# Optimization experiments

Measured on AMD Instinct MI355X. Metric: run time of the kernel, lower is better.

## Reference

```python
import jax, jax.numpy as jnp
import numpy as np

B, S, H = 1, 1024, 2048
E, F, FS = 32, 768, 4096
TOP_K = 4
SCALE = 0.02


def setup_inputs() -> dict:
    key = jax.random.key(0)
    ks = jax.random.split(key, 9)
    return {
        "hidden_states": jax.random.normal(ks[0], (B, S, H), jnp.float32),
        "router_weight": jax.random.normal(ks[1], (E, H), jnp.float32) * SCALE,
        "w_gate": jax.random.normal(ks[2], (E, H, F), jnp.float32) * SCALE,
        "w_up": jax.random.normal(ks[3], (E, H, F), jnp.float32) * SCALE,
        "w_down": jax.random.normal(ks[4], (E, F, H), jnp.float32) * SCALE,
        "sw_gate": jax.random.normal(ks[5], (H, FS), jnp.float32) * SCALE,
        "sw_up": jax.random.normal(ks[6], (H, FS), jnp.float32) * SCALE,
        "sw_down": jax.random.normal(ks[7], (FS, H), jnp.float32) * SCALE,
        "sgate_w": jax.random.normal(ks[8], (H, 1), jnp.float32) * SCALE,
    }


def reference(hidden_states, router_weight, w_gate, w_up, w_down,
              sw_gate, sw_up, sw_down, sgate_w):
    b, s, h = hidden_states.shape
    x = hidden_states.reshape(-1, h)                      # [T,H]
    T = x.shape[0]

    # ---- router: linear -> softmax (fp32) -> topk -> renormalize ----
    logits = x @ router_weight.T                          # [T,E]
    probs = jax.nn.softmax(logits.astype(jnp.float32), axis=-1)
    topv, topi = jax.lax.top_k(probs, TOP_K)              # [T,K]
    topv = topv / jnp.sum(topv, axis=-1, keepdims=True)
    topv = topv.astype(probs.dtype)

    # combine weights: scatter topk weights into dense [T,E] mask
    combine = jnp.zeros((T, E), probs.dtype).at[
        jnp.arange(T)[:, None], topi].add(topv)

    # ---- experts: SwiGLU per expert, weighted combine ----
    g = jnp.einsum('th,ehf->etf', x, w_gate)              # [E,T,F]
    u = jnp.einsum('th,ehf->etf', x, w_up)                # [E,T,F]
    act = jax.nn.silu(g) * u                              # [E,T,F]
    out = jnp.einsum('te,etf,efh->th', combine, act, w_down)  # [T,H]

    # ---- shared expert with sigmoid gate ----
    shared = (jax.nn.silu(x @ sw_gate) * (x @ sw_up)) @ sw_down  # [T,H]
    out = out + jax.nn.sigmoid(x @ sgate_w) * shared

    return out.reshape(b, s, h)
```

## Files before the change

kernel.cpp:

```cpp
#include <hip/hip_runtime.h>
#include <math.h>

#define T_TOK 1024
#define H_DIM 2048
#define N_EXP 32
#define TOPK  4
#define F_DIM 768
#define FS_DIM 4096
#define FS_HALF 2048

typedef __bf16 bf16;
typedef __attribute__((ext_vector_type(2))) __bf16 bf16x2;
typedef __attribute__((ext_vector_type(4))) __bf16 bf16x4;
typedef __attribute__((ext_vector_type(8))) __bf16 bf16x8;
typedef __attribute__((ext_vector_type(4))) float f32x4;

#define BAR() do {                                        \
    asm volatile("s_waitcnt lgkmcnt(0)" ::: "memory");    \
    __builtin_amdgcn_s_barrier();                         \
    __builtin_amdgcn_sched_barrier(0);                    \
  } while (0)

__global__ __launch_bounds__(256) void router_kernel(
    const float* __restrict__ x, const float* __restrict__ rw,
    const float* __restrict__ sgw,
    float* __restrict__ topw, float* __restrict__ sg,
    int* __restrict__ counts, int* __restrict__ lists)
{
  int t = blockIdx.x; int tid = threadIdx.x;
  int lane = tid & 63, wave = tid >> 6;
  float acc[N_EXP];
  #pragma unroll
  for (int e = 0; e < N_EXP; e++) acc[e] = 0.f;
  float accs = 0.f;
  const float* xr = x + (size_t)t * H_DIM;
  for (int h = tid; h < H_DIM; h += 256) {
    float xv = xr[h];
    accs += xv * sgw[h];
    #pragma unroll
    for (int e = 0; e < N_EXP; e++) acc[e] += xv * rw[e * H_DIM + h];
  }
  __shared__ float red[4][N_EXP];
  __shared__ float reds[4];
  __shared__ float logits[N_EXP];
  #pragma unroll
  for (int e = 0; e < N_EXP; e++) {
    float v = acc[e];
    for (int off = 32; off; off >>= 1) v += __shfl_down(v, off, 64);
    if (lane == 0) red[wave][e] = v;
  }
  {
    float v = accs;
    for (int off = 32; off; off >>= 1) v += __shfl_down(v, off, 64);
    if (lane == 0) reds[wave] = v;
  }
  __syncthreads();
  if (tid < N_EXP) logits[tid] = red[0][tid] + red[1][tid] + red[2][tid] + red[3][tid];
  __syncthreads();
  if (tid == 0) {
    float m = -1e30f;
    #pragma unroll
    for (int e = 0; e < N_EXP; e++) m = fmaxf(m, logits[e]);
    float p[N_EXP];
    #pragma unroll
    for (int e = 0; e < N_EXP; e++) p[e] = expf(logits[e] - m);
    int ids[TOPK]; float vs[TOPK]; float wsum = 0.f;
    #pragma unroll
    for (int k = 0; k < TOPK; k++) {
      int best = 0; float bv = -1.f;
      for (int e = 0; e < N_EXP; e++) {
        if (p[e] > bv) { bv = p[e]; best = e; }
      }
      ids[k] = best; vs[k] = bv; wsum += bv; p[best] = -2.f;
    }
    float inv = 1.f / wsum;
    float sgs = reds[0] + reds[1] + reds[2] + reds[3];
    sg[t] = 1.f / (1.f + expf(-sgs));
    #pragma unroll
    for (int k = 0; k < TOPK; k++) {
      int slot = t * TOPK + k;
      topw[slot] = vs[k] * inv;
      int pos = atomicAdd(&counts[ids[k]], 1);
      lists[ids[k] * T_TOK + pos] = slot;
    }
  }
}

__global__ __launch_bounds__(256, 4) void gateup_fused(
    const float* __restrict__ X,
    const float* __restrict__ wg_, const float* __restrict__ wu_,
    const float* __restrict__ swg, const float* __restrict__ swu,
    bf16* __restrict__ act, bf16* __restrict__ acts,
    const int* __restrict__ lists, const int* __restrict__ counts,
    int n_shared, int sh_fbs, int actsN, int col_off)
{
  int id = blockIdx.x;
  bool gather = id >= n_shared;
  const float *Wg, *Wu; const int* lb = nullptr;
  int count, mt, fb, ldb, Nout; bf16* C;
  if (gather) {
    int g = id - n_shared;
    int j = g >> 3;
    int e = (g & 7) + 8 * (j / 96);
    int rr = j % 96;
    fb = (rr % 12) * 64; mt = (rr / 12) * 64;
    count = counts[e]; lb = lists + e * T_TOK;
    Wg = wg_ + (size_t)e * H_DIM * F_DIM;
    Wu = wu_ + (size_t)e * H_DIM * F_DIM;
    ldb = F_DIM; Nout = F_DIM; C = act;
  } else {
    fb = (id % sh_fbs) * 64; mt = (id / sh_fbs) * 64;
    count = T_TOK; ldb = FS_DIM; Nout = actsN;
    Wg = swg + col_off; Wu = swu + col_off;
    C = acts;
  }
  if (mt >= count) return;

  int tid = threadIdx.x;
  int lane = tid & 63, wid = tid >> 6;
  int wr = wid >> 1, wc = wid & 1;

  __shared__ alignas(16) bf16 sA [2][64][40];
  __shared__ alignas(16) bf16 sBg[2][64][40];
  __shared__ alignas(16) bf16 sBu[2][64][40];

  const float* aptr;
  {
    int r = mt + (tid >> 2);
    int rc = r < count ? r : count - 1;
    int tok = gather ? (lb[rc] >> 2) : rc;
    aptr = X + (size_t)tok * H_DIM + ((tid & 3) << 3);
  }
  int tid7 = tid & 127;
  int bk4 = (tid7 >> 4) << 2;
  int bng = tid7 & 15;
  const float* bptr = (tid < 128 ? Wg : Wu) + (size_t)bk4 * ldb + fb + bng * 4;

  f32x4 accg[2][2], accu[2][2];
  #pragma unroll
  for (int m = 0; m < 2; m++)
    #pragma unroll
    for (int n = 0; n < 2; n++) {
      accg[m][n] = (f32x4){0.f,0.f,0.f,0.f};
      accu[m][n] = (f32x4){0.f,0.f,0.f,0.f};
    }

  f32x4 avA[2], bvA[4], avB[2], bvB[4];

  #define ISSUE(av, bv, k0) do {                                      \
    av[0] = *(const f32x4*)(aptr + (k0));                             \
    av[1] = *(const f32x4*)(aptr + (k0) + 4);                         \
    _Pragma("unroll")                                                 \
    for (int r_ = 0; r_ < 4; r_++)                                    \
      bv[r_] = *(const f32x4*)(bptr + (size_t)((k0) + r_) * ldb);     \
  } while (0)

  #define STAGE(b, av, bv) do {                                       \
    bf16x8 t8;                                                        \
    _Pragma("unroll")                                                 \
    for (int j_ = 0; j_ < 4; j_++) {                                  \
      t8[j_] = (bf16)av[0][j_]; t8[4 + j_] = (bf16)av[1][j_];         \
    }                                                                 \
    *(bf16x8*)&sA[b][tid >> 2][(tid & 3) << 3] = t8;                  \
    bf16* bdst_ = (tid < 128) ? &sBg[b][0][0] : &sBu[b][0][0];        \
    _Pragma("unroll")                                                 \
    for (int i_ = 0; i_ < 4; i_++) {                                  \
      bf16x4 tb;                                                      \
      tb[0] = (bf16)bv[0][i_]; tb[1] = (bf16)bv[1][i_];               \
      tb[2] = (bf16)bv[2][i_]; tb[3] = (bf16)bv[3][i_];               \
      *(bf16x4*)(bdst_ + (bng * 4 + i_) * 40 + bk4) = tb;             \
    }                                                                 \
  } while (0)

  #define MFMA_PHASE(b) do {                                          \
    int fc = (lane >> 4) << 3;                                        \
    bf16x8 af0 = *(const bf16x8*)&sA[b][wr * 32 + (lane & 15)][fc];   \
    bf16x8 af1 = *(const bf16x8*)&sA[b][wr * 32 + 16 + (lane & 15)][fc]; \
    _Pragma("unroll")                                                 \
    for (int n_ = 0; n_ < 2; n_++) {                                  \
      int nr = wc * 32 + n_ * 16 + (lane & 15);                       \
      bf16x8 bg = *(const bf16x8*)&sBg[b][nr][fc];                    \
      bf16x8 bu = *(const bf16x8*)&sBu[b][nr][fc];                    \
      accg[0][n_] = __builtin_amdgcn_mfma_f32_16x16x32_bf16(af0, bg, accg[0][n_], 0,0,0); \
      accu[0][n_] = __builtin_amdgcn_mfma_f32_16x16x32_bf16(af0, bu, accu[0][n_], 0,0,0); \
      accg[1][n_] = __builtin_amdgcn_mfma_f32_16x16x32_bf16(af1, bg, accg[1][n_], 0,0,0); \
      accu[1][n_] = __builtin_amdgcn_mfma_f32_16x16x32_bf16(af1, bu, accu[1][n_], 0,0,0); \
    }                                                                 \
  } while (0)

  ISSUE(avA, bvA, 0);
  ISSUE(avB, bvB, 32);
  STAGE(0, avA, bvA);
  BAR();
  const int NT = H_DIM / 32;
  for (int t = 0; t < NT; t += 2) {
    if (t + 2 < NT) ISSUE(avA, bvA, (t + 2) * 32);
    MFMA_PHASE(0);
    STAGE(1, avB, bvB);
    BAR();
    if (t + 3 < NT) ISSUE(avB, bvB, (t + 3) * 32);
    MFMA_PHASE(1);
    if (t + 2 < NT) STAGE(0, avA, bvA);
    BAR();
  }
  #undef ISSUE
  #undef STAGE
  #undef MFMA_PHASE

  #pragma unroll
  for (int m = 0; m < 2; m++) {
    #pragma unroll
    for (int q = 0; q < 4; q++) {
      int gr = mt + wr * 32 + m * 16 + (lane >> 4) * 4 + q;
      if (gr < count) {
        size_t rowo = (gather ? (size_t)lb[gr] : (size_t)gr) * Nout;
        #pragma unroll
        for (int n = 0; n < 2; n++) {
          float g = accg[m][n][q], u = accu[m][n][q];
          C[rowo + fb + wc * 32 + n * 16 + (lane & 15)] =
              (bf16)(g / (1.f + __expf(-g)) * u);
        }
      }
    }
  }
}

__global__ __launch_bounds__(256, 4) void down_fused(
    const bf16* __restrict__ act, const bf16* __restrict__ acts,
    const float* __restrict__ wd_, const float* __restrict__ swd,
    bf16* __restrict__ dslot, float* __restrict__ out,
    const float* __restrict__ sg,
    const int* __restrict__ lists, const int* __restrict__ counts,
    int n_shared, int lda_sh, int kd_sh, int swd_off, int accum)
{
  int id = blockIdx.x;
  bool expert = id >= n_shared;
  const bf16* A; const float* W; const int* lb = nullptr;
  int count, mt, nb, Kd, lda;
  if (expert) {
    int g = id - n_shared;
    int j = g >> 3;
    int e = (g & 7) + 8 * (j >> 8);
    int rr = j & 255;
    nb = (rr & 31) * 64; mt = (rr >> 5) * 64;
    count = counts[e]; lb = lists + e * T_TOK;
    A = act; lda = F_DIM; Kd = F_DIM;
    W = wd_ + (size_t)e * F_DIM * H_DIM;
  } else {
    nb = (id & 31) * 64; mt = (id >> 5) * 64;
    count = T_TOK; A = acts; lda = lda_sh; Kd = kd_sh;
    W = swd + (size_t)swd_off * H_DIM;
  }
  if (mt >= count) return;

  int tid = threadIdx.x;
  int lane = tid & 63, wid = tid >> 6;
  int wr = wid >> 1, wc = wid & 1;

  __shared__ alignas(16) bf16 sA[2][64][40];
  __shared__ alignas(16) bf16 sB[2][64][40];

  const bf16* aptr;
  {
    int r = mt + (tid >> 2);
    int rc = r < count ? r : count - 1;
    int ar = expert ? lb[rc] : rc;
    aptr = A + (size_t)ar * lda + ((tid & 3) << 3);
  }
  int bk2 = (tid >> 4) << 1;
  int bng = tid & 15;
  const float* bptr = W + (size_t)bk2 * H_DIM + nb + bng * 4;

  f32x4 acc[2][2];
  #pragma unroll
  for (int m = 0; m < 2; m++)
    #pragma unroll
    for (int n = 0; n < 2; n++)
      acc[m][n] = (f32x4){0.f,0.f,0.f,0.f};

  uint4 avA, avB; f32x4 bvA[2], bvB[2];

  #define ISSUE(av, bv, k0) do {                                      \
    av = *(const uint4*)(aptr + (k0));                                \
    bv[0] = *(const f32x4*)(bptr + (size_t)(k0) * H_DIM);             \
    bv[1] = *(const f32x4*)(bptr + (size_t)((k0) + 1) * H_DIM);      \
  } while (0)

  #define STAGE(b, av, bv) do {                                       \
    *(uint4*)&sA[b][tid >> 2][(tid & 3) << 3] = av;                   \
    _Pragma("unroll")                                                 \
    for (int i_ = 0; i_ < 4; i_++) {                                  \
      bf16x2 tb;                                                      \
      tb[0] = (bf16)bv[0][i_]; tb[1] = (bf16)bv[1][i_];               \
      *(bf16x2*)&sB[b][bng * 4 + i_][bk2] = tb;                       \
    }                                                                 \
  } while (0)

  #define MFMA_PHASE(b) do {                                          \
    int fc = (lane >> 4) << 3;                                        \
    bf16x8 af0 = *(const bf16x8*)&sA[b][wr * 32 + (lane & 15)][fc];   \
    bf16x8 af1 = *(const bf16x8*)&sA[b][wr * 32 + 16 + (lane & 15)][fc]; \
    _Pragma("unroll")                                                 \
    for (int n_ = 0; n_ < 2; n_++) {                                  \
      bf16x8 bb = *(const bf16x8*)&sB[b][wc * 32 + n_ * 16 + (lane & 15)][fc]; \
      acc[0][n_] = __builtin_amdgcn_mfma_f32_16x16x32_bf16(af0, bb, acc[0][n_], 0,0,0); \
      acc[1][n_] = __builtin_amdgcn_mfma_f32_16x16x32_bf16(af1, bb, acc[1][n_], 0,0,0); \
    }                                                                 \
  } while (0)

  ISSUE(avA, bvA, 0);
  ISSUE(avB, bvB, 32);
  STAGE(0, avA, bvA);
  BAR();
  const int NT = Kd / 32;
  for (int t = 0; t < NT; t += 2) {
    if (t + 2 < NT) ISSUE(avA, bvA, (t + 2) * 32);
    MFMA_PHASE(0);
    STAGE(1, avB, bvB);
    BAR();
    if (t + 3 < NT) ISSUE(avB, bvB, (t + 3) * 32);
    MFMA_PHASE(1);
    if (t + 2 < NT) STAGE(0, avA, bvA);
    BAR();
  }
  #undef ISSUE
  #undef STAGE
  #undef MFMA_PHASE

  #pragma unroll
  for (int m = 0; m < 2; m++) {
    #pragma unroll
    for (int q = 0; q < 4; q++) {
      int gr = mt + wr * 32 + m * 16 + (lane >> 4) * 4 + q;
      if (gr < count) {
        #pragma unroll
        for (int n = 0; n < 2; n++) {
          int col = nb + wc * 32 + n * 16 + (lane & 15);
          if (expert) {
            dslot[(size_t)lb[gr] * H_DIM + col] = (bf16)acc[m][n][q];
          } else if (!accum) {
            out[(size_t)gr * H_DIM + col] = sg[gr] * acc[m][n][q];
          } else {
            out[(size_t)gr * H_DIM + col] += sg[gr] * acc[m][n][q];
          }
        }
      }
    }
  }
}

__global__ __launch_bounds__(256) void combine_kernel(
    const bf16* __restrict__ dslot, const float* __restrict__ topw,
    float* __restrict__ out)
{
  int t = blockIdx.x;
  int h = threadIdx.x * 8;
  float w0 = topw[t * 4 + 0], w1 = topw[t * 4 + 1];
  float w2 = topw[t * 4 + 2], w3 = topw[t * 4 + 3];
  bf16x8 a0 = *(const bf16x8*)&dslot[(size_t)(t * 4 + 0) * H_DIM + h];
  bf16x8 a1 = *(const bf16x8*)&dslot[(size_t)(t * 4 + 1) * H_DIM + h];
  bf16x8 a2 = *(const bf16x8*)&dslot[(size_t)(t * 4 + 2) * H_DIM + h];
  bf16x8 a3 = *(const bf16x8*)&dslot[(size_t)(t * 4 + 3) * H_DIM + h];
  f32x4 o0 = *(f32x4*)&out[(size_t)t * H_DIM + h];
  f32x4 o1 = *(f32x4*)&out[(size_t)t * H_DIM + h + 4];
  float o[8] = {o0[0], o0[1], o0[2], o0[3], o1[0], o1[1], o1[2], o1[3]};
  #pragma unroll
  for (int j = 0; j < 8; j++)
    o[j] += w0 * (float)a0[j] + w1 * (float)a1[j] + w2 * (float)a2[j]
          + w3 * (float)a3[j];
  *(f32x4*)&out[(size_t)t * H_DIM + h]     = (f32x4){o[0], o[1], o[2], o[3]};
  *(f32x4*)&out[(size_t)t * H_DIM + h + 4] = (f32x4){o[4], o[5], o[6], o[7]};
}

extern "C" void kernel_launch(void* const* d_in, const int* in_sizes, int n_in,
                              void* d_out, int out_size, void* d_ws, size_t ws_size,
                              hipStream_t stream) {
  const float* x   = (const float*)d_in[0];
  const float* rw  = (const float*)d_in[1];
  const float* wg  = (const float*)d_in[2];
  const float* wu  = (const float*)d_in[3];
  const float* wd  = (const float*)d_in[4];
  const float* swg = (const float*)d_in[5];
  const float* swu = (const float*)d_in[6];
  const float* swd = (const float*)d_in[7];
  const float* sgw = (const float*)d_in[8];
  float* out = (float*)d_out;
  char* ws = (char*)d_ws;

  bool fullfs = ws_size >= (size_t)31700000;
  size_t actsN = fullfs ? FS_DIM : FS_HALF;

  size_t off = 0;
  int*   counts = (int*)(ws + off); off += 256;
  int*   lists  = (int*)(ws + off); off += (size_t)N_EXP * T_TOK * 4;
  float* topw   = (float*)(ws + off); off += (size_t)T_TOK * TOPK * 4;
  float* sg     = (float*)(ws + off); off += (size_t)T_TOK * 4;
  bf16*  act    = (bf16*)(ws + off); off += (size_t)T_TOK * TOPK * F_DIM * 2;
  bf16*  acts   = (bf16*)(ws + off); off += (size_t)T_TOK * actsN * 2;
  bf16*  dslot  = (bf16*)(ws + off); off += (size_t)T_TOK * TOPK * H_DIM * 2;

  hipMemsetAsync(counts, 0, 256, stream);

  router_kernel<<<T_TOK, 256, 0, stream>>>(x, rw, sgw, topw, sg, counts, lists);

  if (fullfs) {
    int nsh = (FS_DIM / 64) * 16;
    gateup_fused<<<nsh + 3072, 256, 0, stream>>>(
        x, wg, wu, swg, swu, act, acts, lists, counts, nsh, FS_DIM / 64, FS_DIM, 0);
    down_fused<<<512 + 8192, 256, 0, stream>>>(
        act, acts, wd, swd, dslot, out, sg, lists, counts,
        512, FS_DIM, FS_DIM, 0, 0);
  } else {
    int nsh = (FS_HALF / 64) * 16;
    gateup_fused<<<nsh + 3072, 256, 0, stream>>>(
        x, wg, wu, swg, swu, act, acts, lists, counts, nsh, FS_HALF / 64, FS_HALF, 0);
    down_fused<<<512 + 8192, 256, 0, stream>>>(
        act, acts, wd, swd, dslot, out, sg, lists, counts,
        512, FS_HALF, FS_HALF, 0, 0);
    gateup_fused<<<nsh, 256, 0, stream>>>(
        x, wg, wu, swg, swu, act, acts, lists, counts, nsh, FS_HALF / 64, FS_HALF, FS_HALF);
    down_fused<<<512, 256, 0, stream>>>(
        act, acts, wd, swd, dslot, out, sg, lists, counts,
        512, FS_HALF, FS_HALF, FS_HALF, 1);
  }
  combine_kernel<<<T_TOK, 256, 0, stream>>>(dslot, topw, out);
}
```

Before: 420.2 us.

## Widen GEMM N-tiles to 128, swizzle LDS, single-buffer register prefetch, setprio MFMA

Both the gate/up and down GEMM kernels move from 64x64 to 64x128 output tiles, with grid math and launch counts halved to match. This doubles A-tile reuse per block and cuts redundant activation loads. Padded LDS arrays are replaced with an XOR-swizzled 64-byte-row layout to avoid bank conflicts without padding. The two-stage register prefetch is simplified to a single register set per iteration, and the MFMA phases are wrapped in s_setprio. The cost is more accumulator registers (occupancy hint lowered from 4 to 3 waves) and fewer, larger blocks, which may hurt load balance across sparse expert tiles.

```diff
diff --git a/kernel.cpp b/kernel.cpp
--- a/kernel.cpp
+++ b/kernel.cpp
@@ -10,7 +10,6 @@
 #define FS_HALF 2048
 
 typedef __bf16 bf16;
-typedef __attribute__((ext_vector_type(2))) __bf16 bf16x2;
 typedef __attribute__((ext_vector_type(4))) __bf16 bf16x4;
 typedef __attribute__((ext_vector_type(8))) __bf16 bf16x8;
 typedef __attribute__((ext_vector_type(4))) float f32x4;
@@ -20,6 +19,10 @@
     __builtin_amdgcn_s_barrier();                         \
     __builtin_amdgcn_sched_barrier(0);                    \
   } while (0)
+
+__device__ __forceinline__ int swz(int row, int colB) {
+  return row * 64 + (colB ^ (((row >> 2) & 3) << 4));
+}
 
 __global__ __launch_bounds__(256) void router_kernel(
     const float* __restrict__ x, const float* __restrict__ rw,
@@ -86,7 +89,7 @@
   }
 }
 
-__global__ __launch_bounds__(256, 4) void gateup_fused(
+__global__ __launch_bounds__(256, 3) void gateup_fused(
     const float* __restrict__ X,
     const float* __restrict__ wg_, const float* __restrict__ wu_,
     const float* __restrict__ swg, const float* __restrict__ swu,
@@ -101,15 +104,15 @@
   if (gather) {
     int g = id - n_shared;
     int j = g >> 3;
-    int e = (g & 7) + 8 * (j / 96);
-    int rr = j % 96;
-    fb = (rr % 12) * 64; mt = (rr / 12) * 64;
+    int e = (g & 7) + 8 * (j / 48);
+    int rr = j % 48;
+    fb = (rr % 6) * 128; mt = (rr / 6) * 64;
     count = counts[e]; lb = lists + e * T_TOK;
     Wg = wg_ + (size_t)e * H_DIM * F_DIM;
     Wu = wu_ + (size_t)e * H_DIM * F_DIM;
     ldb = F_DIM; Nout = F_DIM; C = act;
   } else {
-    fb = (id % sh_fbs) * 64; mt = (id / sh_fbs) * 64;
+    fb = (id % sh_fbs) * 128; mt = (id / sh_fbs) * 64;
     count = T_TOK; ldb = FS_DIM; Nout = actsN;
     Wg = swg + col_off; Wu = swu + col_off;
     C = acts;
@@ -120,9 +123,9 @@
   int lane = tid & 63, wid = tid >> 6;
   int wr = wid >> 1, wc = wid & 1;
 
-  __shared__ alignas(16) bf16 sA [2][64][40];
-  __shared__ alignas(16) bf16 sBg[2][64][40];
-  __shared__ alignas(16) bf16 sBu[2][64][40];
+  __shared__ alignas(16) char sA [2][64 * 64];
+  __shared__ alignas(16) char sBg[2][128 * 64];
+  __shared__ alignas(16) char sBu[2][128 * 64];
 
   const float* aptr;
   {
@@ -131,78 +134,79 @@
     int tok = gather ? (lb[rc] >> 2) : rc;
     aptr = X + (size_t)tok * H_DIM + ((tid & 3) << 3);
   }
-  int tid7 = tid & 127;
-  int bk4 = (tid7 >> 4) << 2;
-  int bng = tid7 & 15;
-  const float* bptr = (tid < 128 ? Wg : Wu) + (size_t)bk4 * ldb + fb + bng * 4;
-
-  f32x4 accg[2][2], accu[2][2];
+  int bng = tid & 31;
+  int bk4 = (tid >> 5) << 2;
+  const float* bgp = Wg + (size_t)bk4 * ldb + fb + bng * 4;
+  const float* bup = Wu + (size_t)bk4 * ldb + fb + bng * 4;
+
+  f32x4 accg[2][4], accu[2][4];
   #pragma unroll
   for (int m = 0; m < 2; m++)
     #pragma unroll
-    for (int n = 0; n < 2; n++) {
+    for (int n = 0; n < 4; n++) {
       accg[m][n] = (f32x4){0.f,0.f,0.f,0.f};
       accu[m][n] = (f32x4){0.f,0.f,0.f,0.f};
     }
 
-  f32x4 avA[2], bvA[4], avB[2], bvB[4];
-
-  #define ISSUE(av, bv, k0) do {                                      \
-    av[0] = *(const f32x4*)(aptr + (k0));                             \
-    av[1] = *(const f32x4*)(aptr + (k0) + 4);                         \
-    _Pragma("unroll")                                                 \
-    for (int r_ = 0; r_ < 4; r_++)                                    \
-      bv[r_] = *(const f32x4*)(bptr + (size_t)((k0) + r_) * ldb);     \
-  } while (0)
-
-  #define STAGE(b, av, bv) do {                                       \
+  f32x4 av0, av1, gv[4], uv[4];
+
+  #define ISSUE(k0) do {                                              \
+    av0 = *(const f32x4*)(aptr + (k0));                               \
+    av1 = *(const f32x4*)(aptr + (k0) + 4);                           \
+    _Pragma("unroll")                                                 \
+    for (int r_ = 0; r_ < 4; r_++) {                                  \
+      gv[r_] = *(const f32x4*)(bgp + (size_t)((k0) + r_) * ldb);      \
+      uv[r_] = *(const f32x4*)(bup + (size_t)((k0) + r_) * ldb);      \
+    } } while (0)
+
+  #define STAGE(b) do {                                               \
     bf16x8 t8;                                                        \
     _Pragma("unroll")                                                 \
     for (int j_ = 0; j_ < 4; j_++) {                                  \
-      t8[j_] = (bf16)av[0][j_]; t8[4 + j_] = (bf16)av[1][j_];         \
+      t8[j_] = (bf16)av0[j_]; t8[4 + j_] = (bf16)av1[j_];             \
     }                                                                 \
-    *(bf16x8*)&sA[b][tid >> 2][(tid & 3) << 3] = t8;                  \
-    bf16* bdst_ = (tid < 128) ? &sBg[b][0][0] : &sBu[b][0][0];        \
+    *(bf16x8*)(sA[b] + swz(tid >> 2, (tid & 3) << 4)) = t8;           \
     _Pragma("unroll")                                                 \
     for (int i_ = 0; i_ < 4; i_++) {                                  \
-      bf16x4 tb;                                                      \
-      tb[0] = (bf16)bv[0][i_]; tb[1] = (bf16)bv[1][i_];               \
-      tb[2] = (bf16)bv[2][i_]; tb[3] = (bf16)bv[3][i_];               \
-      *(bf16x4*)(bdst_ + (bng * 4 + i_) * 40 + bk4) = tb;             \
-    }                                                                 \
-  } while (0)
+      bf16x4 tg, tu;                                                  \
+      tg[0] = (bf16)gv[0][i_]; tg[1] = (bf16)gv[1][i_];               \
+      tg[2] = (bf16)gv[2][i_]; tg[3] = (bf16)gv[3][i_];               \
+      tu[0] = (bf16)uv[0][i_]; tu[1] = (bf16)uv[1][i_];               \
+      tu[2] = (bf16)uv[2][i_]; tu[3] = (bf16)uv[3][i_];               \
+      *(bf16x4*)(sBg[b] + swz(bng * 4 + i_, bk4 << 1)) = tg;          \
+      *(bf16x4*)(sBu[b] + swz(bng * 4 + i_, bk4 << 1)) = tu;          \
+    } } while (0)
 
   #define MFMA_PHASE(b) do {                                          \
-    int fc = (lane >> 4) << 3;                                        \
-    bf16x8 af0 = *(const bf16x8*)&sA[b][wr * 32 + (lane & 15)][fc];   \
-    bf16x8 af1 = *(const bf16x8*)&sA[b][wr * 32 + 16 + (lane & 15)][fc]; \
-    _Pragma("unroll")                                                 \
-    for (int n_ = 0; n_ < 2; n_++) {                                  \
-      int nr = wc * 32 + n_ * 16 + (lane & 15);                       \
-      bf16x8 bg = *(const bf16x8*)&sBg[b][nr][fc];                    \
-      bf16x8 bu = *(const bf16x8*)&sBu[b][nr][fc];                    \
+    __builtin_amdgcn_s_setprio(1);                                    \
+    int l15 = lane & 15, qB = (lane >> 4) << 4;                       \
+    bf16x8 af0 = *(const bf16x8*)(sA[b] + swz(wr * 32 + l15, qB));    \
+    bf16x8 af1 = *(const bf16x8*)(sA[b] + swz(wr * 32 + 16 + l15, qB)); \
+    _Pragma("unroll")                                                 \
+    for (int n_ = 0; n_ < 4; n_++) {                                  \
+      int rb = wc * 64 + n_ * 16 + l15;                               \
+      bf16x8 bg = *(const bf16x8*)(sBg[b] + swz(rb, qB));             \
+      bf16x8 bu = *(const bf16x8*)(sBu[b] + swz(rb, qB));             \
       accg[0][n_] = __builtin_amdgcn_mfma_f32_16x16x32_bf16(af0, bg, accg[0][n_], 0,0,0); \
+      accg[1][n_] = __builtin_amdgcn_mfma_f32_16x16x32_bf16(af1, bg, accg[1][n_], 0,0,0); \
       accu[0][n_] = __builtin_amdgcn_mfma_f32_16x16x32_bf16(af0, bu, accu[0][n_], 0,0,0); \
-      accg[1][n_] = __builtin_amdgcn_mfma_f32_16x16x32_bf16(af1, bg, accg[1][n_], 0,0,0); \
       accu[1][n_] = __builtin_amdgcn_mfma_f32_16x16x32_bf16(af1, bu, accu[1][n_], 0,0,0); \
     }                                                                 \
+    __builtin_amdgcn_s_setprio(0);                                    \
   } while (0)
 
-  ISSUE(avA, bvA, 0);
-  ISSUE(avB, bvB, 32);
-  STAGE(0, avA, bvA);
+  const int NT = H_DIM / 32;
+  ISSUE(0);
+  STAGE(0);
+  ISSUE(32);
   BAR();
-  const int NT = H_DIM / 32;
-  for (int t = 0; t < NT; t += 2) {
-    if (t + 2 < NT) ISSUE(avA, bvA, (t + 2) * 32);
-    MFMA_PHASE(0);
-    STAGE(1, avB, bvB);
+  for (int t = 0; t < NT - 1; ++t) {
+    MFMA_PHASE(t & 1);
+    STAGE((t + 1) & 1);
+    if (t + 2 < NT) ISSUE((t + 2) * 32);
     BAR();
-    if (t + 3 < NT) ISSUE(avB, bvB, (t + 3) * 32);
-    MFMA_PHASE(1);
-    if (t + 2 < NT) STAGE(0, avA, bvA);
-    BAR();
-  }
+  }
+  MFMA_PHASE((NT - 1) & 1);
   #undef ISSUE
   #undef STAGE
   #undef MFMA_PHASE
@@ -215,9 +219,9 @@
       if (gr < count) {
         size_t rowo = (gather ? (size_t)lb[gr] : (size_t)gr) * Nout;
         #pragma unroll
-        for (int n = 0; n < 2; n++) {
+        for (int n = 0; n < 4; n++) {
           float g = accg[m][n][q], u = accu[m][n][q];
-          C[rowo + fb + wc * 32 + n * 16 + (lane & 15)] =
+          C[rowo + fb + wc * 64 + n * 16 + (lane & 15)] =
               (bf16)(g / (1.f + __expf(-g)) * u);
         }
       }
@@ -240,14 +244,14 @@
   if (expert) {
     int g = id - n_shared;
     int j = g >> 3;
-    int e = (g & 7) + 8 * (j >> 8);
-    int rr = j & 255;
-    nb = (rr & 31) * 64; mt = (rr >> 5) * 64;
+    int e = (g & 7) + 8 * (j >> 7);
+    int rr = j & 127;
+    nb = (rr & 15) * 128; mt = (rr >> 4) * 64;
     count = counts[e]; lb = lists + e * T_TOK;
     A = act; lda = F_DIM; Kd = F_DIM;
     W = wd_ + (size_t)e * F_DIM * H_DIM;
   } else {
-    nb = (id & 31) * 64; mt = (id >> 5) * 64;
+    nb = (id & 15) * 128; mt = (id >> 4) * 64;
     count = T_TOK; A = acts; lda = lda_sh; Kd = kd_sh;
     W = swd + (size_t)swd_off * H_DIM;
   }
@@ -257,8 +261,8 @@
   int lane = tid & 63, wid = tid >> 6;
   int wr = wid >> 1, wc = wid & 1;
 
-  __shared__ alignas(16) bf16 sA[2][64][40];
-  __shared__ alignas(16) bf16 sB[2][64][40];
+  __shared__ alignas(16) char sA[2][64 * 64];
+  __shared__ alignas(16) char sB[2][128 * 64];
 
   const bf16* aptr;
   {
@@ -267,62 +271,62 @@
     int ar = expert ? lb[rc] : rc;
     aptr = A + (size_t)ar * lda + ((tid & 3) << 3);
   }
-  int bk2 = (tid >> 4) << 1;
-  int bng = tid & 15;
-  const float* bptr = W + (size_t)bk2 * H_DIM + nb + bng * 4;
-
-  f32x4 acc[2][2];
+  int bng = tid & 31;
+  int bk4 = (tid >> 5) << 2;
+  const float* bptr = W + (size_t)bk4 * H_DIM + nb + bng * 4;
+
+  f32x4 acc[2][4];
   #pragma unroll
   for (int m = 0; m < 2; m++)
     #pragma unroll
-    for (int n = 0; n < 2; n++)
+    for (int n = 0; n < 4; n++)
       acc[m][n] = (f32x4){0.f,0.f,0.f,0.f};
 
-  uint4 avA, avB; f32x4 bvA[2], bvB[2];
-
-  #define ISSUE(av, bv, k0) do {                                      \
-    av = *(const uint4*)(aptr + (k0));                                \
-    bv[0] = *(const f32x4*)(bptr + (size_t)(k0) * H_DIM);             \
-    bv[1] = *(const f32x4*)(bptr + (size_t)((k0) + 1) * H_DIM);      \
-  } while (0)
-
-  #define STAGE(b, av, bv) do {                                       \
-    *(uint4*)&sA[b][tid >> 2][(tid & 3) << 3] = av;                   \
+  f32x4 av, bv[4];
+
+  #define ISSUE(k0) do {                                              \
+    av = *(const f32x4*)(aptr + (k0));                                \
+    _Pragma("unroll")                                                 \
+    for (int r_ = 0; r_ < 4; r_++)                                    \
+      bv[r_] = *(const f32x4*)(bptr + (size_t)((k0) + r_) * H_DIM);   \
+    } while (0)
+
+  #define STAGE(b) do {                                               \
+    *(f32x4*)(sA[b] + swz(tid >> 2, (tid & 3) << 4)) = av;            \
     _Pragma("unroll")                                                 \
     for (int i_ = 0; i_ < 4; i_++) {                                  \
-      bf16x2 tb;                                                      \
+      bf16x4 tb;                                                      \
       tb[0] = (bf16)bv[0][i_]; tb[1] = (bf16)bv[1][i_];               \
-      *(bf16x2*)&sB[b][bng * 4 + i_][bk2] = tb;                       \
-    }                                                                 \
-  } while (0)
+      tb[2] = (bf16)bv[2][i_]; tb[3] = (bf16)bv[3][i_];               \
+      *(bf16x4*)(sB[b] + swz(bng * 4 + i_, bk4 << 1)) = tb;           \
+    } } while (0)
 
   #define MFMA_PHASE(b) do {                                          \
-    int fc = (lane >> 4) << 3;                                        \
-    bf16x8 af0 = *(const bf16x8*)&sA[b][wr * 32 + (lane & 15)][fc];   \
-    bf16x8 af1 = *(const bf16x8*)&sA[b][wr * 32 + 16 + (lane & 15)][fc]; \
-    _Pragma("unroll")                                                 \
-    for (int n_ = 0; n_ < 2; n_++) {                                  \
-      bf16x8 bb = *(const bf16x8*)&sB[b][wc * 32 + n_ * 16 + (lane & 15)][fc]; \
+    __builtin_amdgcn_s_setprio(1);                                    \
+    int l15 = lane & 15, qB = (lane >> 4) << 4;                       \
+    bf16x8 af0 = *(const bf16x8*)(sA[b] + swz(wr * 32 + l15, qB));    \
+    bf16x8 af1 = *(const bf16x8*)(sA[b] + swz(wr * 32 + 16 + l15, qB)); \
+    _Pragma("unroll")                                                 \
+    for (int n_ = 0; n_ < 4; n_++) {                                  \
+      bf16x8 bb = *(const bf16x8*)(sB[b] + swz(wc * 64 + n_ * 16 + l15, qB)); \
       acc[0][n_] = __builtin_amdgcn_mfma_f32_16x16x32_bf16(af0, bb, acc[0][n_], 0,0,0); \
       acc[1][n_] = __builtin_amdgcn_mfma_f32_16x16x32_bf16(af1, bb, acc[1][n_], 0,0,0); \
     }                                                                 \
+    __builtin_amdgcn_s_setprio(0);                                    \
   } while (0)
 
-  ISSUE(avA, bvA, 0);
-  ISSUE(avB, bvB, 32);
-  STAGE(0, avA, bvA);
+  const int NT = Kd / 32;
+  ISSUE(0);
+  STAGE(0);
+  ISSUE(32);
   BAR();
-  const int NT = Kd / 32;
-  for (int t = 0; t < NT; t += 2) {
-    if (t + 2 < NT) ISSUE(avA, bvA, (t + 2) * 32);
-    MFMA_PHASE(0);
-    STAGE(1, avB, bvB);
+  for (int t = 0; t < NT - 1; ++t) {
+    MFMA_PHASE(t & 1);
+    STAGE((t + 1) & 1);
+    if (t + 2 < NT) ISSUE((t + 2) * 32);
     BAR();
-    if (t + 3 < NT) ISSUE(avB, bvB, (t + 3) * 32);
-    MFMA_PHASE(1);
-    if (t + 2 < NT) STAGE(0, avA, bvA);
-    BAR();
-  }
+  }
+  MFMA_PHASE((NT - 1) & 1);
   #undef ISSUE
   #undef STAGE
   #undef MFMA_PHASE
@@ -334,8 +338,8 @@
       int gr = mt + wr * 32 + m * 16 + (lane >> 4) * 4 + q;
       if (gr < count) {
         #pragma unroll
-        for (int n = 0; n < 2; n++) {
-          int col = nb + wc * 32 + n * 16 + (lane & 15);
+        for (int n = 0; n < 4; n++) {
+          int col = nb + wc * 64 + n * 16 + (lane & 15);
           if (expert) {
             dslot[(size_t)lb[gr] * H_DIM + col] = (bf16)acc[m][n][q];
           } else if (!accum) {
@@ -403,25 +407,27 @@
 
   router_kernel<<<T_TOK, 256, 0, stream>>>(x, rw, sgw, topw, sg, counts, lists);
 
+  const int EXP_GU = N_EXP * 48;
+  const int EXP_DN = N_EXP * 128;
   if (fullfs) {
-    int nsh = (FS_DIM / 64) * 16;
-    gateup_fused<<<nsh + 3072, 256, 0, stream>>>(
-        x, wg, wu, swg, swu, act, acts, lists, counts, nsh, FS_DIM / 64, FS_DIM, 0);
-    down_fused<<<512 + 8192, 256, 0, stream>>>(
+    int nsh = 16 * (FS_DIM / 128);
+    gateup_fused<<<nsh + EXP_GU, 256, 0, stream>>>(
+        x, wg, wu, swg, swu, act, acts, lists, counts, nsh, FS_DIM / 128, FS_DIM, 0);
+    down_fused<<<256 + EXP_DN, 256, 0, stream>>>(
         act, acts, wd, swd, dslot, out, sg, lists, counts,
-        512, FS_DIM, FS_DIM, 0, 0);
+        256, FS_DIM, FS_DIM, 0, 0);
   } else {
-    int nsh = (FS_HALF / 64) * 16;
-    gateup_fused<<<nsh + 3072, 256, 0, stream>>>(
-        x, wg, wu, swg, swu, act, acts, lists, counts, nsh, FS_HALF / 64, FS_HALF, 0);
-    down_fused<<<512 + 8192, 256, 0, stream>>>(
+    int nsh = 16 * (FS_HALF / 128);
+    gateup_fused<<<nsh + EXP_GU, 256, 0, stream>>>(
+        x, wg, wu, swg, swu, act, acts, lists, counts, nsh, FS_HALF / 128, FS_HALF, 0);
+    down_fused<<<256 + EXP_DN, 256, 0, stream>>>(
         act, acts, wd, swd, dslot, out, sg, lists, counts,
-        512, FS_HALF, FS_HALF, 0, 0);
+        256, FS_HALF, FS_HALF, 0, 0);
     gateup_fused<<<nsh, 256, 0, stream>>>(
-        x, wg, wu, swg, swu, act, acts, lists, counts, nsh, FS_HALF / 64, FS_HALF, FS_HALF);
-    down_fused<<<512, 256, 0, stream>>>(
+        x, wg, wu, swg, swu, act, acts, lists, counts, nsh, FS_HALF / 128, FS_HALF, FS_HALF);
+    down_fused<<<256, 256, 0, stream>>>(
         act, acts, wd, swd, dslot, out, sg, lists, counts,
-        512, FS_HALF, FS_HALF, FS_HALF, 1);
+        256, FS_HALF, FS_HALF, FS_HALF, 1);
   }
   combine_kernel<<<T_TOK, 256, 0, stream>>>(dslot, topw, out);
 }
```

Result: faster. 380.4 us (-9.5%).
